# Performance work log

Measured on AMD Instinct MI355X. Metric: run time of the kernel, lower is better.

The kernel has to match this reference:

```python
import jax, jax.numpy as jnp
import numpy as np

BATCH = 4096
FEATURES = 64
VOCAB = 580000
EMB_DIM = 32
MODELS = 512
SEQ_LEN = 128


def _positional_encoding(position, d_model):
    # Faithful to the numpy get_angles: 1/10000^(2*(i//2)/d_model), sin on even, cos on odd.
    pos = jnp.arange(position, dtype=jnp.float32)[:, None]          # [P, 1]
    i = jnp.arange(d_model, dtype=jnp.float32)[None, :]             # [1, D]
    angle_rates = 1.0 / jnp.power(10000.0, (2.0 * jnp.floor(i / 2.0)) / jnp.float32(d_model))
    angles = pos * angle_rates                                      # [P, D]
    even = (jnp.arange(d_model) % 2 == 0)[None, :]
    pe = jnp.where(even, jnp.sin(angles), jnp.cos(angles))
    return pe[None]                                                 # [1, P, D]


def setup_inputs() -> dict:
    key = jax.random.key(0)
    k1, k2, k3 = jax.random.split(key, 3)
    tokens = jax.random.randint(k1, (BATCH, FEATURES), 0, VOCAB, dtype=jnp.int32)
    emb_table = jax.random.normal(k2, (VOCAB, EMB_DIM), dtype=jnp.float32)
    W = jax.random.normal(k3, (FEATURES * EMB_DIM, MODELS), dtype=jnp.float32) * 0.02
    b = jnp.zeros((MODELS,), dtype=jnp.float32)
    return {"tokens": tokens, "emb_table": emb_table, "W": W, "b": b}


def reference(tokens, emb_table, W, b):
    B, F = tokens.shape
    # gather + scale by sqrt(models)
    x = emb_table[tokens] * jnp.sqrt(jnp.float32(MODELS))           # [B, F, E]
    x = x.reshape(B, F * EMB_DIM)                                   # [B, F*E]
    x = x @ W + b                                                   # [B, M]
    # tf.tile(row, [seq_len]) then reshape (seq_len, models) == broadcast over seq axis
    pe = _positional_encoding(SEQ_LEN, MODELS)                      # [1, S, M]
    out = x[:, None, :] + pe[:, :SEQ_LEN, :]                        # [B, S, M]
    return out
```

## Files before the change

### kernel.cpp

```cpp
#include <hip/hip_runtime.h>
#include <math.h>

#define BATCH   4096
#define FEAT    64
#define EMB     32
#define MODELS  512
#define SEQ     128
#define KDIM    (FEAT * EMB)

#define SQRT_MODELS 22.62741699796952f
#define LN10000     9.210340371976184f

typedef __attribute__((ext_vector_type(4))) float        f32x4;
typedef __attribute__((ext_vector_type(8))) short        bf16x8;
typedef __attribute__((ext_vector_type(4))) unsigned int u32x4;

#define WT_BYTES  ((size_t)MODELS * KDIM * 2)
#define PE_BYTES  ((size_t)SEQ * MODELS * 4)
#define X_BYTES   ((size_t)BATCH * MODELS * 4)
#define ABF_BYTES ((size_t)BATCH * KDIM * 2)
#define WS_MID    (WT_BYTES + PE_BYTES + X_BYTES)
#define WS_FULL   (WT_BYTES + PE_BYTES + X_BYTES + ABF_BYTES)

__device__ inline unsigned short bf16_rne(float f) {
    unsigned int b = __builtin_bit_cast(unsigned int, f);
    return (unsigned short)((b + 0x7FFFu + ((b >> 16) & 1u)) >> 16);
}

#define CVT_PK4(pk, v0, v1)                                                     \
    {                                                                           \
        unsigned int q0, q1, q2, q3;                                            \
        asm("v_cvt_pk_bf16_f32 %0, %1, %2" : "=v"(q0) : "v"(v0.x), "v"(v0.y));  \
        asm("v_cvt_pk_bf16_f32 %0, %1, %2" : "=v"(q1) : "v"(v0.z), "v"(v0.w));  \
        asm("v_cvt_pk_bf16_f32 %0, %1, %2" : "=v"(q2) : "v"(v1.x), "v"(v1.y));  \
        asm("v_cvt_pk_bf16_f32 %0, %1, %2" : "=v"(q3) : "v"(v1.z), "v"(v1.w));  \
        pk = (u32x4){q0, q1, q2, q3};                                           \
    }

__global__ __launch_bounds__(256)
void prep_all(const int* __restrict__ tokens, const float* __restrict__ emb,
              const float* __restrict__ W, const float* __restrict__ bias,
              unsigned short* __restrict__ Wt, float* __restrict__ pe,
              unsigned short* __restrict__ Abf) {
    const int bx  = blockIdx.x;
    const int tid = threadIdx.x;

    if (bx < 1024) {
        __shared__ float t[32][33];
        const int k0 = (bx & 63) * 32;
        const int n0 = (bx >> 6) * 32;
        const int tx = tid & 31;
        const int ty = tid >> 5;
        #pragma unroll
        for (int i = 0; i < 4; ++i)
            t[ty + i * 8][tx] = W[(size_t)(k0 + ty + i * 8) * MODELS + n0 + tx] * SQRT_MODELS;
        __syncthreads();
        #pragma unroll
        for (int i = 0; i < 4; ++i)
            Wt[(size_t)(n0 + ty + i * 8) * KDIM + k0 + tx] = bf16_rne(t[tx][ty + i * 8]);
    } else if (bx < 1280) {
        const int idx = (bx - 1024) * 256 + tid;
        const int s = idx >> 9;
        const int m = idx & (MODELS - 1);
        const float rate = expf(-LN10000 * (float)(2 * (m >> 1)) * (1.0f / 512.0f));
        const float ang  = (float)s * rate;
        pe[idx] = ((m & 1) ? cosf(ang) : sinf(ang)) + bias[m];
    } else {
        const int g    = (bx - 1280) * 256 + tid;
        const int fr   = g >> 2;
        const int part = g & 3;
        const int tok  = tokens[fr];
        const float* src = emb + (size_t)tok * EMB + part * 8;
        const f32x4 v0 = *(const f32x4*)src;
        const f32x4 v1 = *(const f32x4*)(src + 4);
        u32x4 pk;
        CVT_PK4(pk, v0, v1);
        *(u32x4*)(Abf + (size_t)g * 8) = pk;
    }
}

__global__ __launch_bounds__(512)
void gemm_dense8(const unsigned short* __restrict__ Abf,
                 const unsigned short* __restrict__ Wt,
                 float* __restrict__ x) {
    const int tid  = threadIdx.x;
    const int lane = tid & 63;
    const int wave = tid >> 6;
    const int ln   = lane & 15;
    const int kg   = lane >> 4;
    const int m0 = blockIdx.y * 64 + (wave & 3) * 16;
    const int n0 = blockIdx.x * 64 + (wave >> 2) * 32;

    const unsigned short* ap  = Abf + (size_t)(m0 + ln) * KDIM + kg * 8;
    const unsigned short* b0p = Wt  + (size_t)(n0 + ln) * KDIM + kg * 8;
    const unsigned short* b1p = b0p + 16 * KDIM;

    f32x4 acc0 = {0,0,0,0}, acc1 = {0,0,0,0};

    #pragma unroll 4
    for (int k = 0; k < KDIM; k += 32) {
        const bf16x8 a  = *(const bf16x8*)(ap + k);
        const bf16x8 b0 = *(const bf16x8*)(b0p + k);
        const bf16x8 b1 = *(const bf16x8*)(b1p + k);
        acc0 = __builtin_amdgcn_mfma_f32_16x16x32_bf16(a, b0, acc0, 0, 0, 0);
        acc1 = __builtin_amdgcn_mfma_f32_16x16x32_bf16(a, b1, acc1, 0, 0, 0);
    }
    #pragma unroll
    for (int q = 0; q < 4; ++q) {
        const int r = kg * 4 + q;
        x[(size_t)(m0 + r) * MODELS + n0 + ln]      = acc0[q];
        x[(size_t)(m0 + r) * MODELS + n0 + 16 + ln] = acc1[q];
    }
}

__global__ __launch_bounds__(256)
void bcast_pe(const float* __restrict__ x, const float* __restrict__ pe,
              float* __restrict__ out) {
    const int tid = threadIdx.x;
    const int m4  = tid & 127;
    const int b   = blockIdx.x * 2 + (tid >> 7);
    const f32x4 xv = *(const f32x4*)(x + (size_t)b * MODELS + m4 * 4);
    const f32x4* pev = (const f32x4*)pe;
    float* ob = out + (size_t)b * SEQ * MODELS + m4 * 4;
    #pragma unroll 8
    for (int s = 0; s < SEQ; ++s) {
        const f32x4 p = pev[s * 128 + m4];
        __builtin_nontemporal_store(xv + p, (f32x4*)(ob + (size_t)s * MODELS));
    }
}

__global__ __launch_bounds__(256)
void gemm_mfma(const int* __restrict__ tokens, const float* __restrict__ emb,
               const unsigned short* __restrict__ Wt, float* __restrict__ x) {
    const int tid  = threadIdx.x;
    const int wave = tid >> 6;
    const int lane = tid & 63;
    const int ln   = lane & 15;
    const int kg   = lane >> 4;
    const int m_base = blockIdx.y * 16;
    const int n_base = blockIdx.x * 256 + wave * 64;
    const int* trow = tokens + (size_t)(m_base + ln) * FEAT;
    const unsigned short* bptr[4];
    #pragma unroll
    for (int nf = 0; nf < 4; ++nf)
        bptr[nf] = Wt + (size_t)(n_base + nf * 16 + ln) * KDIM + kg * 8;
    f32x4 acc[4] = {f32x4{0,0,0,0}, f32x4{0,0,0,0}, f32x4{0,0,0,0}, f32x4{0,0,0,0}};
    for (int f4 = 0; f4 < FEAT; f4 += 4) {
        const int4 tok4 = *(const int4*)(trow + f4);
        const int toks[4] = {tok4.x, tok4.y, tok4.z, tok4.w};
        #pragma unroll
        for (int j = 0; j < 4; ++j) {
            const int f = f4 + j;
            const float* ea = emb + (size_t)toks[j] * EMB + kg * 8;
            const f32x4 a0 = *(const f32x4*)ea;
            const f32x4 a1 = *(const f32x4*)(ea + 4);
            u32x4 pk;
            CVT_PK4(pk, a0, a1);
            const bf16x8 afrag = __builtin_bit_cast(bf16x8, pk);
            #pragma unroll
            for (int nf = 0; nf < 4; ++nf) {
                const bf16x8 bfrag = *(const bf16x8*)(bptr[nf] + (size_t)f * EMB);
                acc[nf] = __builtin_amdgcn_mfma_f32_16x16x32_bf16(afrag, bfrag, acc[nf], 0, 0, 0);
            }
        }
    }
    #pragma unroll
    for (int nf = 0; nf < 4; ++nf)
        #pragma unroll
        for (int q = 0; q < 4; ++q)
            x[(size_t)(m_base + kg * 4 + q) * MODELS + n_base + nf * 16 + ln] = acc[nf][q];
}

__global__ __launch_bounds__(256)
void prep_wt(const float* __restrict__ W, unsigned short* __restrict__ Wt) {
    __shared__ float t[32][33];
    const int k0 = blockIdx.x * 32;
    const int n0 = blockIdx.y * 32;
    const int tx = threadIdx.x;
    const int ty = threadIdx.y;
    #pragma unroll
    for (int i = 0; i < 4; ++i)
        t[ty + i * 8][tx] = W[(size_t)(k0 + ty + i * 8) * MODELS + n0 + tx] * SQRT_MODELS;
    __syncthreads();
    #pragma unroll
    for (int i = 0; i < 4; ++i)
        Wt[(size_t)(n0 + ty + i * 8) * KDIM + k0 + tx] = bf16_rne(t[tx][ty + i * 8]);
}

__global__ __launch_bounds__(256)
void prep_pe(const float* __restrict__ bias, float* __restrict__ pe) {
    const int idx = blockIdx.x * 256 + threadIdx.x;
    const int s = idx >> 9;
    const int m = idx & (MODELS - 1);
    const float rate = expf(-LN10000 * (float)(2 * (m >> 1)) * (1.0f / 512.0f));
    const float ang  = (float)s * rate;
    pe[idx] = ((m & 1) ? cosf(ang) : sinf(ang)) + bias[m];
}

#define BM 64
#define BN 64
#define BK 32
__global__ __launch_bounds__(256, 2)
void fused_emb_gemm_pe(const int* __restrict__ tokens, const float* __restrict__ emb,
                       const float* __restrict__ W, const float* __restrict__ bias,
                       float* __restrict__ out) {
    __shared__ float As[BK][BM];
    __shared__ float Bs[BK][BN];
    __shared__ float peS[SEQ][BN];
    const int tid  = threadIdx.x;
    const int bn   = blockIdx.x * BN;
    const int brow = blockIdx.y * BM;
    for (int idx = tid; idx < SEQ * BN; idx += 256) {
        const int s  = idx >> 6;
        const int ml = idx & 63;
        const int m  = bn + ml;
        const float rate = expf(-LN10000 * (float)(2 * (m >> 1)) * (1.0f / 512.0f));
        const float ang  = (float)s * rate;
        peS[s][ml] = (m & 1) ? cosf(ang) : sinf(ang);
    }
    float acc[4][4] = {};
    const int tx = tid & 15;
    const int ty = tid >> 4;
    const int lr = tid >> 2;
    const int lj = tid & 3;
    const int bk = tid >> 4;
    const int bc = (tid & 15) * 4;
    for (int kt = 0; kt < FEAT; ++kt) {
        __syncthreads();
        {
            const int tok = tokens[(brow + lr) * FEAT + kt];
            const float* erow = emb + (size_t)tok * EMB + lj * 8;
            const float4 a0 = *(const float4*)(erow);
            const float4 a1 = *(const float4*)(erow + 4);
            const int k0 = lj * 8;
            As[k0 + 0][lr] = a0.x * SQRT_MODELS; As[k0 + 1][lr] = a0.y * SQRT_MODELS;
            As[k0 + 2][lr] = a0.z * SQRT_MODELS; As[k0 + 3][lr] = a0.w * SQRT_MODELS;
            As[k0 + 4][lr] = a1.x * SQRT_MODELS; As[k0 + 5][lr] = a1.y * SQRT_MODELS;
            As[k0 + 6][lr] = a1.z * SQRT_MODELS; As[k0 + 7][lr] = a1.w * SQRT_MODELS;
        }
        {
            const float* w0 = W + (size_t)(kt * 32 + bk) * MODELS + bn + bc;
            const float* w1 = W + (size_t)(kt * 32 + bk + 16) * MODELS + bn + bc;
            *(float4*)&Bs[bk][bc]      = *(const float4*)w0;
            *(float4*)&Bs[bk + 16][bc] = *(const float4*)w1;
        }
        __syncthreads();
        #pragma unroll
        for (int k = 0; k < BK; ++k) {
            const float4 a = *(const float4*)&As[k][ty * 4];
            const float4 b = *(const float4*)&Bs[k][tx * 4];
            acc[0][0] += a.x * b.x; acc[0][1] += a.x * b.y; acc[0][2] += a.x * b.z; acc[0][3] += a.x * b.w;
            acc[1][0] += a.y * b.x; acc[1][1] += a.y * b.y; acc[1][2] += a.y * b.z; acc[1][3] += a.y * b.w;
            acc[2][0] += a.z * b.x; acc[2][1] += a.z * b.y; acc[2][2] += a.z * b.z; acc[2][3] += a.z * b.w;
            acc[3][0] += a.w * b.x; acc[3][1] += a.w * b.y; acc[3][2] += a.w * b.z; acc[3][3] += a.w * b.w;
        }
    }
    {
        const float4 bv = *(const float4*)(bias + bn + tx * 4);
        #pragma unroll
        for (int i = 0; i < 4; ++i) {
            acc[i][0] += bv.x; acc[i][1] += bv.y; acc[i][2] += bv.z; acc[i][3] += bv.w;
        }
    }
    size_t rowbase[4];
    #pragma unroll
    for (int i = 0; i < 4; ++i)
        rowbase[i] = ((size_t)(brow + ty * 4 + i) * SEQ) * MODELS + bn + tx * 4;
    #pragma unroll 4
    for (int s = 0; s < SEQ; ++s) {
        const float4 pv = *(const float4*)&peS[s][tx * 4];
        const size_t soff = (size_t)s * MODELS;
        #pragma unroll
        for (int i = 0; i < 4; ++i) {
            float4 o;
            o.x = acc[i][0] + pv.x; o.y = acc[i][1] + pv.y;
            o.z = acc[i][2] + pv.z; o.w = acc[i][3] + pv.w;
            *(float4*)(out + rowbase[i] + soff) = o;
        }
    }
}

extern "C" void kernel_launch(void* const* d_in, const int* in_sizes, int n_in,
                              void* d_out, int out_size, void* d_ws, size_t ws_size,
                              hipStream_t stream) {
    const int*   tokens = (const int*)d_in[0];
    const float* emb    = (const float*)d_in[1];
    const float* W      = (const float*)d_in[2];
    const float* bias   = (const float*)d_in[3];
    float*       out    = (float*)d_out;

    if (ws_size >= WS_FULL) {
        char* w = (char*)d_ws;
        unsigned short* Wt  = (unsigned short*)w;
        float*          pe  = (float*)(w + WT_BYTES);
        float*          x   = (float*)(w + WT_BYTES + PE_BYTES);
        unsigned short* Abf = (unsigned short*)(w + WT_BYTES + PE_BYTES + X_BYTES);

        prep_all<<<dim3(1024 + 256 + 4096), dim3(256), 0, stream>>>(
            tokens, emb, W, bias, Wt, pe, Abf);
        gemm_dense8<<<dim3(MODELS / 64, BATCH / 64), dim3(512), 0, stream>>>(Abf, Wt, x);
        bcast_pe<<<dim3(BATCH / 2), dim3(256), 0, stream>>>(x, pe, out);
    } else if (ws_size >= WS_MID) {
        char* w = (char*)d_ws;
        unsigned short* Wt = (unsigned short*)w;
        float* pe = (float*)(w + WT_BYTES);
        float* x  = (float*)(w + WT_BYTES + PE_BYTES);

        prep_wt<<<dim3(KDIM / 32, MODELS / 32), dim3(32, 8), 0, stream>>>(W, Wt);
        prep_pe<<<dim3(SEQ * MODELS / 256), dim3(256), 0, stream>>>(bias, pe);
        gemm_mfma<<<dim3(MODELS / 256, BATCH / 16), dim3(256), 0, stream>>>(tokens, emb, Wt, x);
        bcast_pe<<<dim3(BATCH / 2), dim3(256), 0, stream>>>(x, pe, out);
    } else {
        fused_emb_gemm_pe<<<dim3(MODELS / BN, BATCH / BM), dim3(256), 0, stream>>>(
            tokens, emb, W, bias, out);
    }
}
```

Measured before the change: 302.9 us.

## Fuse GEMM with positional-encoding broadcast via shared-memory staging

Replaces the separate dense GEMM and broadcast kernels with one kernel in which each 512-thread block computes a 16x512 tile of x, stages it in shared memory, and then writes the 128-step broadcast with the PE added. This removes the x round trip through global memory and one kernel launch. In exchange, the GEMM tiling changes: each block now reads all of Wt (the weight matrix) for only 16 rows, so weight reuse per block is lower. Only 256 blocks are launched, and the broadcast write phase is serialized behind the GEMM inside each block.

```diff
diff --git a/kernel.cpp b/kernel.cpp
--- a/kernel.cpp
+++ b/kernel.cpp
@@ -79,53 +79,65 @@
     }
 }
 
+#define XS_STRIDE 516
+
 __global__ __launch_bounds__(512)
-void gemm_dense8(const unsigned short* __restrict__ Abf,
-                 const unsigned short* __restrict__ Wt,
-                 float* __restrict__ x) {
+void gemm_bcast_abf(const unsigned short* __restrict__ Abf,
+                    const unsigned short* __restrict__ Wt,
+                    const float* __restrict__ pe,
+                    float* __restrict__ out) {
+    __shared__ float xs[16 * XS_STRIDE];
+
     const int tid  = threadIdx.x;
+    const int wave = tid >> 6;
     const int lane = tid & 63;
-    const int wave = tid >> 6;
     const int ln   = lane & 15;
     const int kg   = lane >> 4;
-    const int m0 = blockIdx.y * 64 + (wave & 3) * 16;
-    const int n0 = blockIdx.x * 64 + (wave >> 2) * 32;
-
-    const unsigned short* ap  = Abf + (size_t)(m0 + ln) * KDIM + kg * 8;
-    const unsigned short* b0p = Wt  + (size_t)(n0 + ln) * KDIM + kg * 8;
-    const unsigned short* b1p = b0p + 16 * KDIM;
-
-    f32x4 acc0 = {0,0,0,0}, acc1 = {0,0,0,0};
+
+    const int m0     = blockIdx.x * 16;
+    const int n_base = wave * 64;
+
+    const unsigned short* ap = Abf + (size_t)(m0 + ln) * KDIM + kg * 8;
+    const unsigned short* bp = Wt  + (size_t)(n_base + ln) * KDIM + kg * 8;
+
+    f32x4 acc[4] = {f32x4{0,0,0,0}, f32x4{0,0,0,0}, f32x4{0,0,0,0}, f32x4{0,0,0,0}};
 
     #pragma unroll 4
     for (int k = 0; k < KDIM; k += 32) {
-        const bf16x8 a  = *(const bf16x8*)(ap + k);
-        const bf16x8 b0 = *(const bf16x8*)(b0p + k);
-        const bf16x8 b1 = *(const bf16x8*)(b1p + k);
-        acc0 = __builtin_amdgcn_mfma_f32_16x16x32_bf16(a, b0, acc0, 0, 0, 0);
-        acc1 = __builtin_amdgcn_mfma_f32_16x16x32_bf16(a, b1, acc1, 0, 0, 0);
-    }
-    #pragma unroll
-    for (int q = 0; q < 4; ++q) {
-        const int r = kg * 4 + q;
-        x[(size_t)(m0 + r) * MODELS + n0 + ln]      = acc0[q];
-        x[(size_t)(m0 + r) * MODELS + n0 + 16 + ln] = acc1[q];
-    }
-}
-
-__global__ __launch_bounds__(256)
-void bcast_pe(const float* __restrict__ x, const float* __restrict__ pe,
-              float* __restrict__ out) {
-    const int tid = threadIdx.x;
-    const int m4  = tid & 127;
-    const int b   = blockIdx.x * 2 + (tid >> 7);
-    const f32x4 xv = *(const f32x4*)(x + (size_t)b * MODELS + m4 * 4);
-    const f32x4* pev = (const f32x4*)pe;
-    float* ob = out + (size_t)b * SEQ * MODELS + m4 * 4;
-    #pragma unroll 8
+        const bf16x8 a = *(const bf16x8*)(ap + k);
+        #pragma unroll
+        for (int nf = 0; nf < 4; ++nf) {
+            const bf16x8 b = *(const bf16x8*)(bp + (size_t)nf * 16 * KDIM + k);
+            acc[nf] = __builtin_amdgcn_mfma_f32_16x16x32_bf16(a, b, acc[nf], 0, 0, 0);
+        }
+    }
+
+    #pragma unroll
+    for (int nf = 0; nf < 4; ++nf)
+        #pragma unroll
+        for (int q = 0; q < 4; ++q)
+            xs[(kg * 4 + q) * XS_STRIDE + n_base + nf * 16 + ln] = acc[nf][q];
+
+    __syncthreads();
+
+    const int r = tid >> 5;
+    const int c = (tid & 31) * 4;
+
+    f32x4 xv[4];
+    #pragma unroll
+    for (int p = 0; p < 4; ++p)
+        xv[p] = *(const f32x4*)&xs[r * XS_STRIDE + p * 128 + c];
+
+    float* ob = out + (size_t)(m0 + r) * SEQ * MODELS;
+    const float* peb = pe;
+    #pragma unroll 2
     for (int s = 0; s < SEQ; ++s) {
-        const f32x4 p = pev[s * 128 + m4];
-        __builtin_nontemporal_store(xv + p, (f32x4*)(ob + (size_t)s * MODELS));
+        const size_t so = (size_t)s * MODELS;
+        #pragma unroll
+        for (int p = 0; p < 4; ++p) {
+            const f32x4 pv = *(const f32x4*)(peb + so + p * 128 + c);
+            __builtin_nontemporal_store(xv[p] + pv, (f32x4*)(ob + so + p * 128 + c));
+        }
     }
 }
 
@@ -169,6 +181,22 @@
         #pragma unroll
         for (int q = 0; q < 4; ++q)
             x[(size_t)(m_base + kg * 4 + q) * MODELS + n_base + nf * 16 + ln] = acc[nf][q];
+}
+
+__global__ __launch_bounds__(256)
+void bcast_pe(const float* __restrict__ x, const float* __restrict__ pe,
+              float* __restrict__ out) {
+    const int tid = threadIdx.x;
+    const int m4  = tid & 127;
+    const int b   = blockIdx.x * 2 + (tid >> 7);
+    const f32x4 xv = *(const f32x4*)(x + (size_t)b * MODELS + m4 * 4);
+    const f32x4* pev = (const f32x4*)pe;
+    float* ob = out + (size_t)b * SEQ * MODELS + m4 * 4;
+    #pragma unroll 8
+    for (int s = 0; s < SEQ; ++s) {
+        const f32x4 p = pev[s * 128 + m4];
+        __builtin_nontemporal_store(xv + p, (f32x4*)(ob + (size_t)s * MODELS));
+    }
 }
 
 __global__ __launch_bounds__(256)
@@ -293,13 +321,11 @@
         char* w = (char*)d_ws;
         unsigned short* Wt  = (unsigned short*)w;
         float*          pe  = (float*)(w + WT_BYTES);
-        float*          x   = (float*)(w + WT_BYTES + PE_BYTES);
         unsigned short* Abf = (unsigned short*)(w + WT_BYTES + PE_BYTES + X_BYTES);
 
         prep_all<<<dim3(1024 + 256 + 4096), dim3(256), 0, stream>>>(
             tokens, emb, W, bias, Wt, pe, Abf);
-        gemm_dense8<<<dim3(MODELS / 64, BATCH / 64), dim3(512), 0, stream>>>(Abf, Wt, x);
-        bcast_pe<<<dim3(BATCH / 2), dim3(256), 0, stream>>>(x, pe, out);
+        gemm_bcast_abf<<<dim3(BATCH / 16), dim3(512), 0, stream>>>(Abf, Wt, pe, out);
     } else if (ws_size >= WS_MID) {
         char* w = (char*)d_ws;
         unsigned short* Wt = (unsigned short*)w;
```

After: 322.8 us. 1.07x slower.
